# Kernel optimization log

Measured on AMD Instinct MI355X. Metric: run time of the kernel, lower is better.

Reference implementation:

```python
import jax, jax.numpy as jnp
import numpy as np
import math
from jax import lax

HIDDEN = 512
BETA = 1.0
MAX_ITERATIONS = 5
CONV_THRESH = 1e-4
SCALE = BETA / math.sqrt(HIDDEN)


def setup_inputs() -> dict:
    key = jax.random.key(0)
    ks = jax.random.split(key, 9)
    B, S, H = 4, 2048, HIDDEN
    w = 1.0 / math.sqrt(H)  # roughly nn.Linear init scale
    return {
        "x": jax.random.normal(ks[0], (B, S, H), jnp.float32),
        "Wq": jax.random.normal(ks[1], (H, H), jnp.float32) * w,
        "bq": jax.random.normal(ks[2], (H,), jnp.float32) * w,
        "Wk": jax.random.normal(ks[3], (H, H), jnp.float32) * w,
        "bk": jax.random.normal(ks[4], (H,), jnp.float32) * w,
        "Wv": jax.random.normal(ks[5], (H, H), jnp.float32) * w,
        "bv": jax.random.normal(ks[6], (H,), jnp.float32) * w,
        "Wo": jax.random.normal(ks[7], (H, H), jnp.float32) * w,
        "bo": jax.random.normal(ks[8], (H,), jnp.float32) * w,
    }


def _hopfield_update(state, keys):
    # scores: [B, S, S]
    scores = jnp.einsum('bsh,bth->bst', state, keys) * SCALE
    attn = jax.nn.softmax(scores, axis=-1)
    return jnp.einsum('bst,bth->bsh', attn, keys)


def reference(x, Wq, bq, Wk, bk, Wv, bv, Wo, bo):
    query = x @ Wq.T + bq
    keys = x @ Wk.T + bk
    values = x @ Wv.T + bv

    # Iterative Hopfield loop: torch breaks after the update that converges.
    # We run a fixed-length scan, freezing state once converged (same math).
    def step(carry, _):
        state, converged, iters = carry
        new_state = _hopfield_update(state, keys)
        # global Frobenius norms, matching torch.norm over the whole tensor
        delta = jnp.linalg.norm(new_state - state) / (jnp.linalg.norm(state) + 1e-8)
        active = jnp.logical_not(converged)
        state = jnp.where(active, new_state, state)
        iters = iters + active.astype(jnp.int32)
        converged = converged | (active & (delta < CONV_THRESH))
        return (state, converged, iters), None

    init = (query, jnp.array(False), jnp.array(0, jnp.int32))
    (state, converged, iterations), _ = lax.scan(step, init, None, length=MAX_ITERATIONS)

    # Final readout attention against values
    scores = jnp.einsum('bsh,bth->bst', state, keys) * SCALE
    attn = jax.nn.softmax(scores, axis=-1)
    out = jnp.einsum('bst,bth->bsh', attn, values)
    out = out @ Wo.T + bo  # dropout p=0.0 / eval: identity
    return out, iterations, converged
```

## Files before the change

kernel.cpp:

```cpp
#include <hip/hip_runtime.h>
#include <hip/hip_bf16.h>
#include <math.h>

#define HH 512
#define BB 4
#define SS 2048
#define NN (BB*SS)
#define SCALE_F 0.04419417382415922f
#define THRESH 1e-4f
#define CTL_FLOATS 1024

typedef __attribute__((ext_vector_type(8))) short bf16x8;
typedef __attribute__((ext_vector_type(4))) float f32x4;

struct Ctl { float sum_d; float sum_o; int iters; int conv; int cur; int bf[10]; };

__device__ __forceinline__ float b2f(unsigned short u) {
    union { unsigned int i; float f; } c; c.i = ((unsigned int)u) << 16; return c.f;
}
__device__ __forceinline__ unsigned short f2b(float f) {
    unsigned int x = __float_as_uint(f);
    unsigned int r = (x + 0x7FFFu + ((x >> 16) & 1u)) >> 16;
    return (unsigned short)r;
}
__device__ __forceinline__ void splitf(float x, unsigned short& h, unsigned short& l) {
    h = f2b(x);
    l = f2b(x - b2f(h));
}
__device__ __forceinline__ f32x4 MF(bf16x8 a, bf16x8 b, f32x4 c) {
    return __builtin_amdgcn_mfma_f32_16x16x32_bf16(a, b, c, 0, 0, 0);
}

#define FBAR() do { \
    asm volatile("s_waitcnt lgkmcnt(0)" ::: "memory"); \
    __builtin_amdgcn_s_barrier(); \
    asm volatile("" ::: "memory"); \
} while (0)

#define LD4(R, ph, pl) do { \
    const unsigned short* _ph = (ph); const unsigned short* _pl = (pl); \
    R##0 = *(const uint4*)(_ph); R##1 = *(const uint4*)(_ph + 8); \
    R##2 = *(const uint4*)(_pl); R##3 = *(const uint4*)(_pl + 8); \
} while (0)
#define ST4SW(base, rowv, g0v, R) do { \
    unsigned short* _b = (base); \
    const int _r7 = (rowv) & 7; \
    unsigned short* _d0 = _b + ((((g0v))     ^ _r7) << 3); \
    unsigned short* _d1 = _b + ((((g0v) + 1) ^ _r7) << 3); \
    *(uint4*)_d0 = R##0; *(uint4*)_d1 = R##1; \
    *(uint4*)(_d0 + 8192) = R##2; *(uint4*)(_d1 + 8192) = R##3; \
} while (0)

__global__ __launch_bounds__(256) void detect_dtypes(
        const void* p0, const void* p1, const void* p2, const void* p3, const void* p4,
        const void* p5, const void* p6, const void* p7, const void* p8, Ctl* sc)
{
    const void* ps[9] = {p0,p1,p2,p3,p4,p5,p6,p7,p8};
    const int   ns[9] = {NN*HH, HH*HH, HH, HH*HH, HH, HH*HH, HH, HH*HH, HH};
    const int i = blockIdx.x;
    const unsigned short* u = (const unsigned short*)ps[i];
    const int n = ns[i] < 4096 ? ns[i] : 4096;
    __shared__ int cnt;
    if (threadIdx.x == 0) cnt = 0;
    __syncthreads();
    int c = 0;
    for (int j = threadIdx.x; j < n; j += 256) {
        const int e = (u[j] >> 7) & 0xFF;
        if (e < 32 || e >= 224) ++c;
    }
    if (c) atomicAdd(&cnt, c);
    __syncthreads();
    if (threadIdx.x == 0) sc->bf[i] = (cnt * 16 < n) ? 1 : 0;
}

__global__ __launch_bounds__(64) void init_flags(Ctl* sc) {
    if (threadIdx.x == 0) {
        sc->iters = 0; sc->conv = 0; sc->cur = 0; sc->sum_d = 0.f; sc->sum_o = 0.f;
        int any = 0;
        for (int i = 0; i < 9; ++i) any |= sc->bf[i];
        sc->bf[9] = any;
    }
}

__global__ __launch_bounds__(256) void mfma_gemm(
    const void* __restrict__ Xv, int xIdx,
    const void* __restrict__ Wv, int wIdx,
    const void* __restrict__ Bv, int bIdx,
    float* __restrict__ outF, void* __restrict__ outExt,
    unsigned short* __restrict__ pKH, unsigned short* __restrict__ pKL,
    unsigned short* __restrict__ pKTH, unsigned short* __restrict__ pKTL,
    float* __restrict__ S0w, float* __restrict__ S1w,
    int mode, const Ctl* __restrict__ sc)
{
    __shared__ unsigned short Xh[64][72], Xl[64][72], Wh[64][72], Wl[64][72];
    const int tid = threadIdx.x;
    const int cur = sc->cur;
    const void* Xp = (xIdx == -2) ? (const void*)(cur ? S1w : S0w) : Xv;
    const bool xbf = (xIdx >= 0) && (sc->bf[xIdx] != 0);
    const bool wbf = (sc->bf[wIdx] != 0);
    const bool bbf = (sc->bf[bIdx] != 0);
    const bool obf = (mode == 1) && (sc->bf[9] != 0);
    const bool xs = !xbf, ws = !wbf;

    const int m0 = blockIdx.x * 64, n0 = blockIdx.y * 64;
    const int lane = tid & 63, w = tid >> 6;
    const int mi = w & 1, ni = w >> 1;
    const int quad = lane >> 4, l16 = lane & 15;
    const int srow = tid >> 2, skb = (tid & 3) * 16;

    f32x4 acc[2][2];
    #pragma unroll
    for (int a = 0; a < 2; ++a)
        #pragma unroll
        for (int bq = 0; bq < 2; ++bq) acc[a][bq] = (f32x4){0.f, 0.f, 0.f, 0.f};

    for (int kc = 0; kc < HH; kc += 64) {
        __syncthreads();
        {
            float v[16];
            if (xbf) {
                const unsigned short* p = (const unsigned short*)Xp + (size_t)(m0 + srow)*HH + kc + skb;
                #pragma unroll
                for (int i = 0; i < 4; ++i) {
                    ushort4 t = *(const ushort4*)(p + 4*i);
                    v[4*i]=b2f(t.x); v[4*i+1]=b2f(t.y); v[4*i+2]=b2f(t.z); v[4*i+3]=b2f(t.w);
                }
            } else {
                const float* p = (const float*)Xp + (size_t)(m0 + srow)*HH + kc + skb;
                #pragma unroll
                for (int i = 0; i < 4; ++i) {
                    float4 t = *(const float4*)(p + 4*i);
                    v[4*i]=t.x; v[4*i+1]=t.y; v[4*i+2]=t.z; v[4*i+3]=t.w;
                }
            }
            #pragma unroll
            for (int i = 0; i < 4; ++i) {
                unsigned short h[4], l[4];
                #pragma unroll
                for (int j = 0; j < 4; ++j) splitf(v[4*i+j], h[j], l[j]);
                *(ushort4*)&Xh[srow][skb + 4*i] = make_ushort4(h[0], h[1], h[2], h[3]);
                if (xs) *(ushort4*)&Xl[srow][skb + 4*i] = make_ushort4(l[0], l[1], l[2], l[3]);
            }
        }
        {
            float v[16];
            if (wbf) {
                const unsigned short* p = (const unsigned short*)Wv + (size_t)(n0 + srow)*HH + kc + skb;
                #pragma unroll
                for (int i = 0; i < 4; ++i) {
                    ushort4 t = *(const ushort4*)(p + 4*i);
                    v[4*i]=b2f(t.x); v[4*i+1]=b2f(t.y); v[4*i+2]=b2f(t.z); v[4*i+3]=b2f(t.w);
                }
            } else {
                const float* p = (const float*)Wv + (size_t)(n0 + srow)*HH + kc + skb;
                #pragma unroll
                for (int i = 0; i < 4; ++i) {
                    float4 t = *(const float4*)(p + 4*i);
                    v[4*i]=t.x; v[4*i+1]=t.y; v[4*i+2]=t.z; v[4*i+3]=t.w;
                }
            }
            #pragma unroll
            for (int i = 0; i < 4; ++i) {
                unsigned short h[4], l[4];
                #pragma unroll
                for (int j = 0; j < 4; ++j) splitf(v[4*i+j], h[j], l[j]);
                *(ushort4*)&Wh[srow][skb + 4*i] = make_ushort4(h[0], h[1], h[2], h[3]);
                if (ws) *(ushort4*)&Wl[srow][skb + 4*i] = make_ushort4(l[0], l[1], l[2], l[3]);
            }
        }
        __syncthreads();
        #pragma unroll
        for (int d = 0; d < 2; ++d) {
            const int kl = 32*d + quad*8;
            #pragma unroll
            for (int mt = 0; mt < 2; ++mt) {
                const int xr = 32*mi + 16*mt + l16;
                bf16x8 ahx = *(const bf16x8*)&Xh[xr][kl];
                bf16x8 alx;
                if (xs) alx = *(const bf16x8*)&Xl[xr][kl];
                #pragma unroll
                for (int nt = 0; nt < 2; ++nt) {
                    const int wr = 32*ni + 16*nt + l16;
                    bf16x8 bh = *(const bf16x8*)&Wh[wr][kl];
                    acc[mt][nt] = MF(ahx, bh, acc[mt][nt]);
                    if (xs) acc[mt][nt] = MF(alx, bh, acc[mt][nt]);
                    if (ws) {
                        bf16x8 bl = *(const bf16x8*)&Wl[wr][kl];
                        acc[mt][nt] = MF(ahx, bl, acc[mt][nt]);
                    }
                }
            }
        }
    }
    unsigned short* vtH = nullptr;
    if (mode == 4) { vtH = (unsigned short*)(cur ? S0w : S1w); }
    #pragma unroll
    for (int nt = 0; nt < 2; ++nt) {
        const int col = n0 + 32*ni + 16*nt + l16;
        const float bv = bbf ? b2f(((const unsigned short*)Bv)[col]) : ((const float*)Bv)[col];
        #pragma unroll
        for (int mt = 0; mt < 2; ++mt)
            #pragma unroll
            for (int e = 0; e < 4; ++e) {
                const int row = m0 + 32*mi + 16*mt + quad*4 + e;
                const float vv = acc[mt][nt][e] + bv;
                const size_t idx = (size_t)row*HH + col;
                if (mode == 0) outF[idx] = vv;
                else if (mode == 1) {
                    if (obf) ((unsigned short*)outExt)[idx] = f2b(vv);
                    else     ((float*)outExt)[idx] = vv;
                } else {
                    unsigned short h, l; splitf(vv, h, l);
                    const size_t t = ((size_t)(row >> 11) * HH + col) * SS + (row & 2047);
                    if (mode == 3) {
                        pKH[idx] = h; pKL[idx] = l;
                        pKTH[t] = h;  pKTL[t] = l;
                    } else {
                        vtH[t] = h; vtH[(size_t)NN*HH + t] = l;
                    }
                }
            }
    }
}

template<bool FINAL>
__global__ __launch_bounds__(512, 2) void mfma_attn(
    float* __restrict__ S0w, float* __restrict__ S1w,
    const unsigned short* __restrict__ KH, const unsigned short* __restrict__ KL,
    const unsigned short* __restrict__ KTH, const unsigned short* __restrict__ KTL,
    Ctl* sc)
{
    if constexpr (!FINAL) { if (sc->conv) return; }
    const int cur = sc->cur;
    float* Scur = cur ? S1w : S0w;
    float* Out  = FINAL ? Scur : (cur ? S0w : S1w);
    const unsigned short* VTH = FINAL ? (const unsigned short*)(cur ? S0w : S1w) : KTH;
    const unsigned short* VTL = FINAL ? (VTH + (size_t)NN*HH) : KTL;

    __shared__ __align__(16) unsigned short UB0[16384];
    __shared__ __align__(16) unsigned short UB1[16384];
    __shared__ __align__(16) unsigned short SHl[32*520];
    __shared__ __align__(16) unsigned short Pth[32*72], Ptl[32*72];
    __shared__ __align__(16) float Sld[32*68];
    __shared__ __align__(16) float mld[32], lld[32], ald[32];
    __shared__ float redd[8], redo[8];

    const int tid = threadIdx.x;
    const int lane = tid & 63, w = tid >> 6;
    const int quad = lane >> 4, l16 = lane & 15;
    const int r = w & 1, s = w >> 1;

    const int bid = blockIdx.x;
    const int e8 = bid & 7;
    const int b = e8 >> 1;
    const int q0 = 32 * ((bid >> 3) + 32 * (e8 & 1));

    const size_t bSSHH = (size_t)b * SS * HH;
    const size_t bHHSS = (size_t)b * HH * SS;

    const int key = tid >> 3, hs = (tid & 7) * 16;
    const int gS  = (tid & 7) * 2;
    const int rw = tid >> 2, k1 = (tid & 3) * 16;
    const int gP  = (tid & 3) * 2;

    const unsigned short* pSH = KH + bSSHH + (size_t)key*HH + hs;
    const unsigned short* pSL = KL + bSSHH + (size_t)key*HH + hs;
    const size_t vbase = bHHSS + (size_t)(128*(rw >> 5) + (rw & 31))*SS + k1;
    const unsigned short* pVH = VTH + vbase;
    const unsigned short* pVL = VTL + vbase;

    uint4 Ra0, Ra1, Ra2, Ra3;
    uint4 Rb0, Rb1, Rb2, Rb3;
    LD4(Ra, pSH, pSL);
    LD4(Rb, pSH + 128, pSL + 128);

    bf16x8 ah[16];
    {
        const float* Qr = Scur + ((size_t)b*SS + q0 + 16*r + l16) * HH + quad*8;
        #pragma unroll
        for (int f = 0; f < 16; ++f) {
            float4 v0 = *(const float4*)(Qr + 32*f);
            float4 v1 = *(const float4*)(Qr + 32*f + 4);
            unsigned short h[8], l[8];
            splitf(v0.x,h[0],l[0]); splitf(v0.y,h[1],l[1]); splitf(v0.z,h[2],l[2]); splitf(v0.w,h[3],l[3]);
            splitf(v1.x,h[4],l[4]); splitf(v1.y,h[5],l[5]); splitf(v1.z,h[6],l[6]); splitf(v1.w,h[7],l[7]);
            bf16x8 af;
            #pragma unroll
            for (int j = 0; j < 8; ++j) af[j] = (short)h[j];
            ah[f] = af;
            if (s == 0) {
                unsigned short* d = &SHl[(16*r + l16)*520 + 32*f + quad*8];
                *(ushort4*)(d)     = make_ushort4(l[0], l[1], l[2], l[3]);
                *(ushort4*)(d + 4) = make_ushort4(l[4], l[5], l[6], l[7]);
            }
        }
        if (tid < 32) { mld[tid] = -INFINITY; lld[tid] = 0.f; }
    }

    f32x4 O[8];
    #pragma unroll
    for (int i = 0; i < 8; ++i) O[i] = (f32x4){0.f, 0.f, 0.f, 0.f};

    const int shlbase = (16*r + l16)*520 + quad*8;
    const int gsw = l16 & 7;

    for (int kt = 0; kt < SS/64; ++kt) {
        const size_t so = (size_t)kt*64*HH;
        const size_t po = (size_t)kt*64;
        f32x4 sA = (f32x4){0.f,0.f,0.f,0.f}, sB = (f32x4){0.f,0.f,0.f,0.f};
        #pragma unroll
        for (int c = 0; c < 4; ++c) {
            unsigned short* ub = (c & 1) ? UB1 : UB0;
            if ((c & 1) == 0) {
                ST4SW(ub + key*128, key, gS, Ra);
                if (c == 0) LD4(Ra, pSH + so + 2*128, pSL + so + 2*128);
                else        LD4(Ra, pVH + po, pVL + po);
            } else {
                ST4SW(ub + key*128, key, gS, Rb);
                if (c == 1) LD4(Rb, pSH + so + 3*128, pSL + so + 3*128);
                else        LD4(Rb, pVH + (size_t)32*SS + po, pVL + (size_t)32*SS + po);
            }
            FBAR();
            #pragma unroll
            for (int kf = 0; kf < 4; ++kf) {
                bf16x8 alf = *(const bf16x8*)&SHl[shlbase + c*128 + kf*32];
                const int cc = ((4*kf + quad) ^ gsw) << 3;
                const int rb = (16*s + l16)*128;
                bf16x8 bh = *(const bf16x8*)&ub[rb + cc];
                bf16x8 bl = *(const bf16x8*)&ub[8192 + rb + cc];
                const bf16x8 a = ah[c*4 + kf];
                if (kf & 1) {
                    sB = MF(a, bh, sB); sB = MF(alf, bh, sB); sB = MF(a, bl, sB);
                } else {
                    sA = MF(a, bh, sA); sA = MF(alf, bh, sA); sA = MF(a, bl, sA);
                }
            }
        }
        f32x4 sacc = sA + sB;
        #pragma unroll
        for (int e = 0; e < 4; ++e)
            Sld[(16*r + quad*4 + e)*68 + 16*s + l16] = sacc[e] * SCALE_F;
        FBAR();
        {
            const int row = tid >> 4, sg = tid & 15;
            const float* sr = Sld + row*68 + sg*4;
            float4 x0 = *(const float4*)(sr);
            float mt = fmaxf(fmaxf(x0.x, x0.y), fmaxf(x0.z, x0.w));
            #pragma unroll
            for (int mk = 1; mk < 16; mk <<= 1) mt = fmaxf(mt, __shfl_xor(mt, mk, 16));
            const float mprev = mld[row];
            const float mnew = fmaxf(mprev, mt);
            float p[4];
            p[0]=__expf(x0.x-mnew); p[1]=__expf(x0.y-mnew); p[2]=__expf(x0.z-mnew); p[3]=__expf(x0.w-mnew);
            float ps = p[0]+p[1]+p[2]+p[3];
            #pragma unroll
            for (int mk = 1; mk < 16; mk <<= 1) ps += __shfl_xor(ps, mk, 16);
            const float alpha = __expf(mprev - mnew);
            if (sg == 0) { mld[row] = mnew; lld[row] = lld[row]*alpha + ps; ald[row] = alpha; }
            unsigned short h[4], l[4];
            #pragma unroll
            for (int i = 0; i < 4; ++i) splitf(p[i], h[i], l[i]);
            *(ushort4*)&Pth[row*72 + sg*4] = make_ushort4(h[0],h[1],h[2],h[3]);
            *(ushort4*)&Ptl[row*72 + sg*4] = make_ushort4(l[0],l[1],l[2],l[3]);
        }
        FBAR();
        {
            const float4 av = *(const float4*)&ald[16*r + 4*quad];
            const float a4[4] = {av.x, av.y, av.z, av.w};
            #pragma unroll
            for (int i = 0; i < 8; ++i)
                #pragma unroll
                for (int e = 0; e < 4; ++e) O[i][e] *= a4[e];
        }
        bf16x8 pah[2], pal[2];
        #pragma unroll
        for (int kf = 0; kf < 2; ++kf) {
            pah[kf] = *(const bf16x8*)&Pth[(16*r + l16)*72 + kf*32 + quad*8];
            pal[kf] = *(const bf16x8*)&Ptl[(16*r + l16)*72 + kf*32 + quad*8];
        }
        #pragma unroll
        for (int c = 0; c < 4; ++c) {
            unsigned short* ub = (c & 1) ? UB1 : UB0;
            if ((c & 1) == 0) {
                ST4SW(ub + rw*64, rw, gP, Ra);
                if (c == 0)             LD4(Ra, pVH + (size_t)64*SS + po, pVL + (size_t)64*SS + po);
                else if (kt+1 < SS/64)  LD4(Ra, pSH + so + (size_t)64*HH,
                                             pSL + so + (size_t)64*HH);
            } else {
                ST4SW(ub + rw*64, rw, gP, Rb);
                if (c == 1)             LD4(Rb, pVH + (size_t)96*SS + po, pVL + (size_t)96*SS + po);
                else if (kt+1 < SS/64)  LD4(Rb, pSH + so + (size_t)64*HH + 128,
                                             pSL + so + (size_t)64*HH + 128);
            }
            FBAR();
            #pragma unroll
            for (int nt = 0; nt < 2; ++nt) {
                const int rb = (32*s + 16*nt + l16)*64;
                #pragma unroll
                for (int kf = 0; kf < 2; ++kf) {
                    const int cc = ((4*kf + quad) ^ gsw) << 3;
                    bf16x8 bh = *(const bf16x8*)&ub[rb + cc];
                    bf16x8 bl = *(const bf16x8*)&ub[8192 + rb + cc];
                    O[c*2+nt] = MF(pah[kf], bh, O[c*2+nt]);
                    O[c*2+nt] = MF(pal[kf], bh, O[c*2+nt]);
                    O[c*2+nt] = MF(pah[kf], bl, O[c*2+nt]);
                }
            }
        }
    }
    const float4 lv = *(const float4*)&lld[16*r + 4*quad];
    const float inv[4] = {1.f/lv.x, 1.f/lv.y, 1.f/lv.z, 1.f/lv.w};
    float pd = 0.f, po2 = 0.f;
    #pragma unroll
    for (int c = 0; c < 4; ++c)
        #pragma unroll
        for (int nt = 0; nt < 2; ++nt)
            #pragma unroll
            for (int e = 0; e < 4; ++e) {
                const int row = q0 + 16*r + quad*4 + e;
                const int col = 128*s + 32*c + 16*nt + l16;
                const float nv = O[c*2+nt][e] * inv[e];
                const size_t idx = (size_t)b*SS*HH + (size_t)row*HH + col;
                if constexpr (!FINAL) {
                    const float old = Scur[idx];
                    const float d = nv - old;
                    pd += d*d; po2 += old*old;
                }
                Out[idx] = nv;
            }
    if constexpr (!FINAL) {
        #pragma unroll
        for (int mk = 1; mk < 64; mk <<= 1) {
            pd  += __shfl_xor(pd, mk, 64);
            po2 += __shfl_xor(po2, mk, 64);
        }
        if (lane == 0) { redd[w] = pd; redo[w] = po2; }
        __syncthreads();
        if (tid == 0) {
            float td = 0.f, to = 0.f;
            #pragma unroll
            for (int i = 0; i < 8; ++i) { td += redd[i]; to += redo[i]; }
            atomicAdd(&sc->sum_d, td);
            atomicAdd(&sc->sum_o, to);
        }
    }
}

__global__ __launch_bounds__(64) void flag_update(Ctl* sc) {
    if (threadIdx.x != 0) return;
    if (sc->conv) return;
    sc->cur ^= 1;
    sc->iters += 1;
    const float delta = sqrtf(sc->sum_d) / (sqrtf(sc->sum_o) + 1e-8f);
    if (delta < THRESH) sc->conv = 1;
    sc->sum_d = 0.f; sc->sum_o = 0.f;
}

__global__ __launch_bounds__(64) void write_scalars(const Ctl* sc, void* outv) {
    if (threadIdx.x != 0) return;
    if (sc->bf[9]) {
        unsigned short* o = (unsigned short*)outv;
        o[(size_t)NN*HH]     = f2b((float)sc->iters);
        o[(size_t)NN*HH + 1] = f2b(sc->conv ? 1.0f : 0.0f);
    } else {
        float* o = (float*)outv;
        o[(size_t)NN*HH]     = (float)sc->iters;
        o[(size_t)NN*HH + 1] = sc->conv ? 1.0f : 0.0f;
    }
}

extern "C" void kernel_launch(void* const* d_in, const int* in_sizes, int n_in,
                              void* d_out, int out_size, void* d_ws, size_t ws_size,
                              hipStream_t stream)
{
    const void* x  = d_in[0];
    const void* Wq = d_in[1];
    const void* bq = d_in[2];
    const void* Wk = d_in[3];
    const void* bk = d_in[4];
    const void* Wv = d_in[5];
    const void* bv = d_in[6];
    const void* Wo = d_in[7];
    const void* bo = d_in[8];

    Ctl* sc = (Ctl*)d_ws;
    float* S0 = (float*)d_ws + CTL_FLOATS;
    float* S1 = S0 + (size_t)NN*HH;
    unsigned short* KH  = (unsigned short*)(S1 + (size_t)NN*HH);
    unsigned short* KL  = KH  + (size_t)NN*HH;
    unsigned short* KTH = KL  + (size_t)NN*HH;
    unsigned short* KTL = KTH + (size_t)NN*HH;

    const dim3 ggrid(NN/64, HH/64);
    const int  agrid = 256;

    detect_dtypes<<<9, 256, 0, stream>>>(x, Wq, bq, Wk, bk, Wv, bv, Wo, bo, sc);
    init_flags<<<1, 64, 0, stream>>>(sc);

    mfma_gemm<<<ggrid, 256, 0, stream>>>(x, 0, Wq, 1, bq, 2, S0, nullptr,
                                         nullptr, nullptr, nullptr, nullptr, S0, S1, 0, sc);
    mfma_gemm<<<ggrid, 256, 0, stream>>>(x, 0, Wk, 3, bk, 4, nullptr, nullptr,
                                         KH, KL, KTH, KTL, S0, S1, 3, sc);

    for (int it = 0; it < 5; ++it) {
        mfma_attn<false><<<agrid, 512, 0, stream>>>(S0, S1, KH, KL, KTH, KTL, sc);
        flag_update<<<1, 64, 0, stream>>>(sc);
    }

    mfma_gemm<<<ggrid, 256, 0, stream>>>(x, 0, Wv, 5, bv, 6, nullptr, nullptr,
                                         nullptr, nullptr, nullptr, nullptr, S0, S1, 4, sc);
    mfma_attn<true><<<agrid, 512, 0, stream>>>(S0, S1, KH, KL, KTH, KTL, sc);
    mfma_gemm<<<ggrid, 256, 0, stream>>>(nullptr, -2, Wo, 7, bo, 8, nullptr, d_out,
                                         nullptr, nullptr, nullptr, nullptr, S0, S1, 1, sc);
    if (out_size >= (int)((size_t)NN*HH + 2))
        write_scalars<<<1, 64, 0, stream>>>(sc, d_out);
}
```

Baseline: 1.290 ms.

## Shrink attention query tile to 16 rows with 4 waves and register-held low parts

The attention kernel now processes 16 query rows per block with 256 threads (4 waves) instead of 32 rows with 512 threads, and the grid doubles to 512 blocks. The bf16 low half of the query split is held in registers instead of shared memory, and each thread stages twice as much K/V data per load with a single register set. The aim is more blocks for the 256 CUs and lower LDS use. The cost is that each K/V tile is reused by fewer query rows, which doubles global K/V traffic, and register pressure rises.

```diff
diff --git a/kernel.cpp b/kernel.cpp
--- a/kernel.cpp
+++ b/kernel.cpp
@@ -37,18 +37,24 @@
     asm volatile("" ::: "memory"); \
 } while (0)
 
-#define LD4(R, ph, pl) do { \
+#define LD8(R, ph, pl) do { \
     const unsigned short* _ph = (ph); const unsigned short* _pl = (pl); \
-    R##0 = *(const uint4*)(_ph); R##1 = *(const uint4*)(_ph + 8); \
-    R##2 = *(const uint4*)(_pl); R##3 = *(const uint4*)(_pl + 8); \
+    R##0 = *(const uint4*)(_ph);      R##1 = *(const uint4*)(_ph + 8); \
+    R##2 = *(const uint4*)(_ph + 16); R##3 = *(const uint4*)(_ph + 24); \
+    R##4 = *(const uint4*)(_pl);      R##5 = *(const uint4*)(_pl + 8); \
+    R##6 = *(const uint4*)(_pl + 16); R##7 = *(const uint4*)(_pl + 24); \
 } while (0)
-#define ST4SW(base, rowv, g0v, R) do { \
+#define ST8SW(base, rowv, g0v, R) do { \
     unsigned short* _b = (base); \
     const int _r7 = (rowv) & 7; \
-    unsigned short* _d0 = _b + ((((g0v))     ^ _r7) << 3); \
+    unsigned short* _d0 = _b + ((((g0v) + 0) ^ _r7) << 3); \
     unsigned short* _d1 = _b + ((((g0v) + 1) ^ _r7) << 3); \
+    unsigned short* _d2 = _b + ((((g0v) + 2) ^ _r7) << 3); \
+    unsigned short* _d3 = _b + ((((g0v) + 3) ^ _r7) << 3); \
     *(uint4*)_d0 = R##0; *(uint4*)_d1 = R##1; \
-    *(uint4*)(_d0 + 8192) = R##2; *(uint4*)(_d1 + 8192) = R##3; \
+    *(uint4*)_d2 = R##2; *(uint4*)_d3 = R##3; \
+    *(uint4*)(_d0 + 8192) = R##4; *(uint4*)(_d1 + 8192) = R##5; \
+    *(uint4*)(_d2 + 8192) = R##6; *(uint4*)(_d3 + 8192) = R##7; \
 } while (0)
 
 __global__ __launch_bounds__(256) void detect_dtypes(
@@ -224,7 +230,7 @@
 }
 
 template<bool FINAL>
-__global__ __launch_bounds__(512, 2) void mfma_attn(
+__global__ __launch_bounds__(256, 2) void mfma_attn(
     float* __restrict__ S0w, float* __restrict__ S1w,
     const unsigned short* __restrict__ KH, const unsigned short* __restrict__ KL,
     const unsigned short* __restrict__ KTH, const unsigned short* __restrict__ KTL,
@@ -239,44 +245,37 @@
 
     __shared__ __align__(16) unsigned short UB0[16384];
     __shared__ __align__(16) unsigned short UB1[16384];
-    __shared__ __align__(16) unsigned short SHl[32*520];
-    __shared__ __align__(16) unsigned short Pth[32*72], Ptl[32*72];
-    __shared__ __align__(16) float Sld[32*68];
-    __shared__ __align__(16) float mld[32], lld[32], ald[32];
-    __shared__ float redd[8], redo[8];
+    __shared__ __align__(16) unsigned short Pth[16*72], Ptl[16*72];
+    __shared__ __align__(16) float Sld[16*68];
+    __shared__ __align__(16) float mld[16], lld[16], ald[16];
+    __shared__ float redd[4], redo[4];
 
     const int tid = threadIdx.x;
     const int lane = tid & 63, w = tid >> 6;
     const int quad = lane >> 4, l16 = lane & 15;
-    const int r = w & 1, s = w >> 1;
 
     const int bid = blockIdx.x;
-    const int e8 = bid & 7;
-    const int b = e8 >> 1;
-    const int q0 = 32 * ((bid >> 3) + 32 * (e8 & 1));
+    const int b = bid & 3;
+    const int q0 = 16 * (bid >> 2);
 
     const size_t bSSHH = (size_t)b * SS * HH;
     const size_t bHHSS = (size_t)b * HH * SS;
 
-    const int key = tid >> 3, hs = (tid & 7) * 16;
-    const int gS  = (tid & 7) * 2;
-    const int rw = tid >> 2, k1 = (tid & 3) * 16;
-    const int gP  = (tid & 3) * 2;
+    const int key = tid >> 2, hs = (tid & 3) * 32, gS0 = (tid & 3) * 4;
+    const int rw = tid >> 1, k1 = (tid & 1) * 32, gP0 = (tid & 1) * 4;
 
     const unsigned short* pSH = KH + bSSHH + (size_t)key*HH + hs;
     const unsigned short* pSL = KL + bSSHH + (size_t)key*HH + hs;
-    const size_t vbase = bHHSS + (size_t)(128*(rw >> 5) + (rw & 31))*SS + k1;
-    const unsigned short* pVH = VTH + vbase;
-    const unsigned short* pVL = VTL + vbase;
-
-    uint4 Ra0, Ra1, Ra2, Ra3;
-    uint4 Rb0, Rb1, Rb2, Rb3;
-    LD4(Ra, pSH, pSL);
-    LD4(Rb, pSH + 128, pSL + 128);
-
-    bf16x8 ah[16];
+    const int hid0 = 128*(rw >> 5) + (rw & 31);
+    const unsigned short* pVH = VTH + bHHSS + (size_t)hid0*SS + k1;
+    const unsigned short* pVL = VTL + bHHSS + (size_t)hid0*SS + k1;
+
+    uint4 Ra0, Ra1, Ra2, Ra3, Ra4, Ra5, Ra6, Ra7;
+    LD8(Ra, pSH, pSL);
+
+    bf16x8 ah[16], al[16];
     {
-        const float* Qr = Scur + ((size_t)b*SS + q0 + 16*r + l16) * HH + quad*8;
+        const float* Qr = Scur + ((size_t)b*SS + q0 + l16) * HH + quad*8;
         #pragma unroll
         for (int f = 0; f < 16; ++f) {
             float4 v0 = *(const float4*)(Qr + 32*f);
@@ -284,24 +283,18 @@
             unsigned short h[8], l[8];
             splitf(v0.x,h[0],l[0]); splitf(v0.y,h[1],l[1]); splitf(v0.z,h[2],l[2]); splitf(v0.w,h[3],l[3]);
             splitf(v1.x,h[4],l[4]); splitf(v1.y,h[5],l[5]); splitf(v1.z,h[6],l[6]); splitf(v1.w,h[7],l[7]);
-            bf16x8 af;
-            #pragma unroll
-            for (int j = 0; j < 8; ++j) af[j] = (short)h[j];
-            ah[f] = af;
-            if (s == 0) {
-                unsigned short* d = &SHl[(16*r + l16)*520 + 32*f + quad*8];
-                *(ushort4*)(d)     = make_ushort4(l[0], l[1], l[2], l[3]);
-                *(ushort4*)(d + 4) = make_ushort4(l[4], l[5], l[6], l[7]);
-            }
-        }
-        if (tid < 32) { mld[tid] = -INFINITY; lld[tid] = 0.f; }
+            bf16x8 af, bf;
+            #pragma unroll
+            for (int j = 0; j < 8; ++j) { af[j] = (short)h[j]; bf[j] = (short)l[j]; }
+            ah[f] = af; al[f] = bf;
+        }
+        if (tid < 16) { mld[tid] = -INFINITY; lld[tid] = 0.f; }
     }
 
     f32x4 O[8];
     #pragma unroll
     for (int i = 0; i < 8; ++i) O[i] = (f32x4){0.f, 0.f, 0.f, 0.f};
 
-    const int shlbase = (16*r + l16)*520 + quad*8;
     const int gsw = l16 & 7;
 
     for (int kt = 0; kt < SS/64; ++kt) {
@@ -311,21 +304,15 @@
         #pragma unroll
         for (int c = 0; c < 4; ++c) {
             unsigned short* ub = (c & 1) ? UB1 : UB0;
-            if ((c & 1) == 0) {
-                ST4SW(ub + key*128, key, gS, Ra);
-                if (c == 0) LD4(Ra, pSH + so + 2*128, pSL + so + 2*128);
-                else        LD4(Ra, pVH + po, pVL + po);
-            } else {
-                ST4SW(ub + key*128, key, gS, Rb);
-                if (c == 1) LD4(Rb, pSH + so + 3*128, pSL + so + 3*128);
-                else        LD4(Rb, pVH + (size_t)32*SS + po, pVL + (size_t)32*SS + po);
-            }
+            ST8SW(ub + key*128, key, gS0, Ra);
+            if (c < 3) LD8(Ra, pSH + so + (size_t)(c+1)*128, pSL + so + (size_t)(c+1)*128);
+            else       LD8(Ra, pVH + po, pVL + po);
             FBAR();
             #pragma unroll
             for (int kf = 0; kf < 4; ++kf) {
-                bf16x8 alf = *(const bf16x8*)&SHl[shlbase + c*128 + kf*32];
+                const bf16x8 alf = al[c*4 + kf];
                 const int cc = ((4*kf + quad) ^ gsw) << 3;
-                const int rb = (16*s + l16)*128;
+                const int rb = (16*w + l16)*128;
                 bf16x8 bh = *(const bf16x8*)&ub[rb + cc];
                 bf16x8 bl = *(const bf16x8*)&ub[8192 + rb + cc];
                 const bf16x8 a = ah[c*4 + kf];
@@ -339,7 +326,7 @@
         f32x4 sacc = sA + sB;
         #pragma unroll
         for (int e = 0; e < 4; ++e)
-            Sld[(16*r + quad*4 + e)*68 + 16*s + l16] = sacc[e] * SCALE_F;
+            Sld[(quad*4 + e)*68 + 16*w + l16] = sacc[e] * SCALE_F;
         FBAR();
         {
             const int row = tid >> 4, sg = tid & 15;
@@ -365,7 +352,7 @@
         }
         FBAR();
         {
-            const float4 av = *(const float4*)&ald[16*r + 4*quad];
+            const float4 av = *(const float4*)&ald[4*quad];
             const float a4[4] = {av.x, av.y, av.z, av.w};
             #pragma unroll
             for (int i = 0; i < 8; ++i)
@@ -375,27 +362,21 @@
         bf16x8 pah[2], pal[2];
         #pragma unroll
         for (int kf = 0; kf < 2; ++kf) {
-            pah[kf] = *(const bf16x8*)&Pth[(16*r + l16)*72 + kf*32 + quad*8];
-            pal[kf] = *(const bf16x8*)&Ptl[(16*r + l16)*72 + kf*32 + quad*8];
+            pah[kf] = *(const bf16x8*)&Pth[l16*72 + kf*32 + quad*8];
+            pal[kf] = *(const bf16x8*)&Ptl[l16*72 + kf*32 + quad*8];
         }
         #pragma unroll
         for (int c = 0; c < 4; ++c) {
             unsigned short* ub = (c & 1) ? UB1 : UB0;
-            if ((c & 1) == 0) {
-                ST4SW(ub + rw*64, rw, gP, Ra);
-                if (c == 0)             LD4(Ra, pVH + (size_t)64*SS + po, pVL + (size_t)64*SS + po);
-                else if (kt+1 < SS/64)  LD4(Ra, pSH + so + (size_t)64*HH,
-                                             pSL + so + (size_t)64*HH);
-            } else {
-                ST4SW(ub + rw*64, rw, gP, Rb);
-                if (c == 1)             LD4(Rb, pVH + (size_t)96*SS + po, pVL + (size_t)96*SS + po);
-                else if (kt+1 < SS/64)  LD4(Rb, pSH + so + (size_t)64*HH + 128,
-                                             pSL + so + (size_t)64*HH + 128);
-            }
+            ST8SW(ub + rw*64, rw, gP0, Ra);
+            if (c < 3)              LD8(Ra, pVH + (size_t)(c+1)*32*SS + po,
+                                         pVL + (size_t)(c+1)*32*SS + po);
+            else if (kt+1 < SS/64)  LD8(Ra, pSH + so + (size_t)64*HH,
+                                         pSL + so + (size_t)64*HH);
             FBAR();
             #pragma unroll
             for (int nt = 0; nt < 2; ++nt) {
-                const int rb = (32*s + 16*nt + l16)*64;
+                const int rb = (32*w + 16*nt + l16)*64;
                 #pragma unroll
                 for (int kf = 0; kf < 2; ++kf) {
                     const int cc = ((4*kf + quad) ^ gsw) << 3;
@@ -408,7 +389,7 @@
             }
         }
     }
-    const float4 lv = *(const float4*)&lld[16*r + 4*quad];
+    const float4 lv = *(const float4*)&lld[4*quad];
     const float inv[4] = {1.f/lv.x, 1.f/lv.y, 1.f/lv.z, 1.f/lv.w};
     float pd = 0.f, po2 = 0.f;
     #pragma unroll
@@ -417,8 +398,8 @@
         for (int nt = 0; nt < 2; ++nt)
             #pragma unroll
             for (int e = 0; e < 4; ++e) {
-                const int row = q0 + 16*r + quad*4 + e;
-                const int col = 128*s + 32*c + 16*nt + l16;
+                const int row = q0 + quad*4 + e;
+                const int col = 128*w + 32*c + 16*nt + l16;
                 const float nv = O[c*2+nt][e] * inv[e];
                 const size_t idx = (size_t)b*SS*HH + (size_t)row*HH + col;
                 if constexpr (!FINAL) {
@@ -437,11 +418,8 @@
         if (lane == 0) { redd[w] = pd; redo[w] = po2; }
         __syncthreads();
         if (tid == 0) {
-            float td = 0.f, to = 0.f;
-            #pragma unroll
-            for (int i = 0; i < 8; ++i) { td += redd[i]; to += redo[i]; }
-            atomicAdd(&sc->sum_d, td);
-            atomicAdd(&sc->sum_o, to);
+            atomicAdd(&sc->sum_d, redd[0] + redd[1] + redd[2] + redd[3]);
+            atomicAdd(&sc->sum_o, redo[0] + redo[1] + redo[2] + redo[3]);
         }
     }
 }
@@ -492,7 +470,7 @@
     unsigned short* KTL = KTH + (size_t)NN*HH;
 
     const dim3 ggrid(NN/64, HH/64);
-    const int  agrid = 256;
+    const int  agrid = 512;
 
     detect_dtypes<<<9, 256, 0, stream>>>(x, Wq, bq, Wk, bk, Wv, bv, Wo, bo, sc);
     init_flags<<<1, 64, 0, stream>>>(sc);
@@ -503,13 +481,13 @@
                                          KH, KL, KTH, KTL, S0, S1, 3, sc);
 
     for (int it = 0; it < 5; ++it) {
-        mfma_attn<false><<<agrid, 512, 0, stream>>>(S0, S1, KH, KL, KTH, KTL, sc);
+        mfma_attn<false><<<agrid, 256, 0, stream>>>(S0, S1, KH, KL, KTH, KTL, sc);
         flag_update<<<1, 64, 0, stream>>>(sc);
     }
 
     mfma_gemm<<<ggrid, 256, 0, stream>>>(x, 0, Wv, 5, bv, 6, nullptr, nullptr,
                                          nullptr, nullptr, nullptr, nullptr, S0, S1, 4, sc);
-    mfma_attn<true><<<agrid, 512, 0, stream>>>(S0, S1, KH, KL, KTH, KTL, sc);
+    mfma_attn<true><<<agrid, 256, 0, stream>>>(S0, S1, KH, KL, KTH, KTL, sc);
     mfma_gemm<<<ggrid, 256, 0, stream>>>(nullptr, -2, Wo, 7, bo, 8, nullptr, d_out,
                                          nullptr, nullptr, nullptr, nullptr, S0, S1, 1, sc);
     if (out_size >= (int)((size_t)NN*HH + 2))
```

Result: slower. 2.314 ms (+79.3%).

## Load V operand fragments directly from global memory instead of staging through LDS

Applied to the files above, without the earlier changes.

The PV matmul phase no longer stages V^T tiles through shared memory with barriers. Each wave now reads its bf16 hi/lo V fragments straight from global memory into registers. The register prefetch slots freed this way are used to prefetch the next key tile earlier. This removes LDS stores and four barriers per tile, but each wave now issues uncoalesced, unshared global loads and gets no software prefetch for V.

```diff
diff --git a/kernel.cpp b/kernel.cpp
--- a/kernel.cpp
+++ b/kernel.cpp
@@ -260,14 +260,9 @@
 
     const int key = tid >> 3, hs = (tid & 7) * 16;
     const int gS  = (tid & 7) * 2;
-    const int rw = tid >> 2, k1 = (tid & 3) * 16;
-    const int gP  = (tid & 3) * 2;
 
     const unsigned short* pSH = KH + bSSHH + (size_t)key*HH + hs;
     const unsigned short* pSL = KL + bSSHH + (size_t)key*HH + hs;
-    const size_t vbase = bHHSS + (size_t)(128*(rw >> 5) + (rw & 31))*SS + k1;
-    const unsigned short* pVH = VTH + vbase;
-    const unsigned short* pVL = VTL + vbase;
 
     uint4 Ra0, Ra1, Ra2, Ra3;
     uint4 Rb0, Rb1, Rb2, Rb3;
@@ -306,6 +301,7 @@
 
     for (int kt = 0; kt < SS/64; ++kt) {
         const size_t so = (size_t)kt*64*HH;
+        const size_t son = ((kt+1 < SS/64) ? (size_t)(kt+1)*64*HH : 0);
         const size_t po = (size_t)kt*64;
         f32x4 sA = (f32x4){0.f,0.f,0.f,0.f}, sB = (f32x4){0.f,0.f,0.f,0.f};
         #pragma unroll
@@ -314,11 +310,11 @@
             if ((c & 1) == 0) {
                 ST4SW(ub + key*128, key, gS, Ra);
                 if (c == 0) LD4(Ra, pSH + so + 2*128, pSL + so + 2*128);
-                else        LD4(Ra, pVH + po, pVL + po);
+                else        LD4(Ra, pSH + son,        pSL + son);
             } else {
                 ST4SW(ub + key*128, key, gS, Rb);
                 if (c == 1) LD4(Rb, pSH + so + 3*128, pSL + so + 3*128);
-                else        LD4(Rb, pVH + (size_t)32*SS + po, pVL + (size_t)32*SS + po);
+                else        LD4(Rb, pSH + son + 128,  pSL + son + 128);
             }
             FBAR();
             #pragma unroll
@@ -380,32 +376,24 @@
         }
         #pragma unroll
         for (int c = 0; c < 4; ++c) {
-            unsigned short* ub = (c & 1) ? UB1 : UB0;
-            if ((c & 1) == 0) {
-                ST4SW(ub + rw*64, rw, gP, Ra);
-                if (c == 0)             LD4(Ra, pVH + (size_t)64*SS + po, pVL + (size_t)64*SS + po);
-                else if (kt+1 < SS/64)  LD4(Ra, pSH + so + (size_t)64*HH,
-                                             pSL + so + (size_t)64*HH);
-            } else {
-                ST4SW(ub + rw*64, rw, gP, Rb);
-                if (c == 1)             LD4(Rb, pVH + (size_t)96*SS + po, pVL + (size_t)96*SS + po);
-                else if (kt+1 < SS/64)  LD4(Rb, pSH + so + (size_t)64*HH + 128,
-                                             pSL + so + (size_t)64*HH + 128);
-            }
-            FBAR();
-            #pragma unroll
-            for (int nt = 0; nt < 2; ++nt) {
-                const int rb = (32*s + 16*nt + l16)*64;
+            bf16x8 vh[2][2], vl[2][2];
+            #pragma unroll
+            for (int nt = 0; nt < 2; ++nt)
                 #pragma unroll
                 for (int kf = 0; kf < 2; ++kf) {
-                    const int cc = ((4*kf + quad) ^ gsw) << 3;
-                    bf16x8 bh = *(const bf16x8*)&ub[rb + cc];
-                    bf16x8 bl = *(const bf16x8*)&ub[8192 + rb + cc];
-                    O[c*2+nt] = MF(pah[kf], bh, O[c*2+nt]);
-                    O[c*2+nt] = MF(pal[kf], bh, O[c*2+nt]);
-                    O[c*2+nt] = MF(pah[kf], bl, O[c*2+nt]);
-                }
-            }
+                    const size_t g = bHHSS + (size_t)(128*s + 32*c + 16*nt + l16)*SS
+                                   + po + kf*32 + quad*8;
+                    vh[nt][kf] = *(const bf16x8*)(VTH + g);
+                    vl[nt][kf] = *(const bf16x8*)(VTL + g);
+                }
+            #pragma unroll
+            for (int nt = 0; nt < 2; ++nt)
+                #pragma unroll
+                for (int kf = 0; kf < 2; ++kf) {
+                    O[c*2+nt] = MF(pah[kf], vh[nt][kf], O[c*2+nt]);
+                    O[c*2+nt] = MF(pal[kf], vh[nt][kf], O[c*2+nt]);
+                    O[c*2+nt] = MF(pah[kf], vl[nt][kf], O[c*2+nt]);
+                }
         }
     }
     const float4 lv = *(const float4*)&lld[16*r + 4*quad];
```

Result: slower. 2.267 ms (+75.7%).
